# Kernel optimization log

Hardware: AMD Instinct MI355X
Metric: run time of the kernel (lower is better)

Reference implementation:

```python
import jax, jax.numpy as jnp
import numpy as np

N_QUBITS = 7
N_LAYERS = 2
DIM = 2 ** N_QUBITS  # 128
NORM_FACTOR = 1.0


def _cnot_gather_idx(n):
    # CNOT chain (0,1),(1,2),...,(n-2,n-1) plus wraparound (n-1,0).
    # new_state[x] = old_state[idx[x]]; apply gates in reverse to arange.
    gates = [(i, i + 1) for i in range(n - 1)] + [(n - 1, 0)]
    idx = np.arange(2 ** n)
    for c, t in reversed(gates):
        cbit = 1 << (n - 1 - c)  # pennylane wire 0 = most significant bit
        tbit = 1 << (n - 1 - t)
        idx = np.where((idx & cbit) > 0, idx ^ tbit, idx)
    return jnp.asarray(idx)

CNOT_IDX = _cnot_gather_idx(N_QUBITS)


def silu(x):
    return x * jax.nn.sigmoid(x)


def cayley(A_real, A_imag):
    # Hermitianize then Cayley transform -> unitary, per layer. [L,D,D]
    A = A_real.astype(jnp.complex64) + 1j * A_imag.astype(jnp.complex64)
    A = A + jnp.conj(jnp.swapaxes(A, -1, -2))
    I = jnp.eye(DIM, dtype=A.dtype)
    return jnp.matmul(A - 1j * I, jnp.linalg.inv(A + 1j * I))


def _single_qubit_gate(theta_x, theta_y):
    # combined G = RY(theta_y) @ RX(theta_x) applied to every qubit
    cx, sx = jnp.cos(theta_x / 2), jnp.sin(theta_x / 2)
    cy, sy = jnp.cos(theta_y / 2), jnp.sin(theta_y / 2)
    RX = jnp.stack([jnp.stack([cx + 0j, -1j * sx]), jnp.stack([-1j * sx, cx + 0j])])
    RY = jnp.stack([jnp.stack([cy + 0j, -sy + 0j]), jnp.stack([sy + 0j, cy + 0j])])
    return RY @ RX


def quantum_evolve(psi, coeffs, q_mats):
    # psi: [N, DIM] complex64 normalized state vectors
    N = psi.shape[0]
    for j in range(N_LAYERS):
        psi = psi @ q_mats[j].T  # QubitUnitary: new = U @ old
        G = _single_qubit_gate(coeffs[j, 0], coeffs[j, 1])
        psi = psi.reshape((N,) + (2,) * N_QUBITS)
        for ax in range(1, N_QUBITS + 1):
            psi = jnp.moveaxis(jnp.tensordot(G, psi, axes=((1,), (ax,))), 0, ax)
        psi = psi.reshape(N, DIM)
        psi = psi[:, CNOT_IDX]  # CNOT chain is a fixed basis permutation
    return psi


def setup_inputs() -> dict:
    key = jax.random.key(0)
    ks = jax.random.split(key, 16)
    N, E = 50000, 800000
    in_nf, hid, out_nf = 128, 128, 128
    h = jax.random.normal(ks[0], (N, in_nf), dtype=jnp.float32)
    edge_index = jax.random.randint(ks[1], (2, E), 0, N)
    s = 0.05
    W_e1 = jax.random.normal(ks[2], (2 * in_nf, hid), dtype=jnp.float32) * s
    b_e1 = jnp.zeros((hid,), dtype=jnp.float32)
    W_e2 = jax.random.normal(ks[3], (hid, hid), dtype=jnp.float32) * s
    b_e2 = jnp.zeros((hid,), dtype=jnp.float32)
    W_enc = jax.random.normal(ks[4], (hid + in_nf, DIM), dtype=jnp.float32) * s
    b_enc = jnp.zeros((DIM,), dtype=jnp.float32)
    coeffs = jax.random.normal(ks[5], (N_LAYERS, 2), dtype=jnp.float32) * 0.1
    A_real = jax.random.normal(ks[6], (N_LAYERS, DIM, DIM), dtype=jnp.float32) * 0.01
    A_imag = jax.random.normal(ks[7], (N_LAYERS, DIM, DIM), dtype=jnp.float32) * 0.01
    W_dec = jax.random.normal(ks[8], (DIM, out_nf), dtype=jnp.float32) * s
    b_dec = jnp.zeros((out_nf,), dtype=jnp.float32)
    return {"h": h, "edge_index": edge_index, "W_e1": W_e1, "b_e1": b_e1,
            "W_e2": W_e2, "b_e2": b_e2, "W_enc": W_enc, "b_enc": b_enc,
            "coeffs": coeffs, "A_real": A_real, "A_imag": A_imag,
            "W_dec": W_dec, "b_dec": b_dec}


def reference(h, edge_index, W_e1, b_e1, W_e2, b_e2, W_enc, b_enc,
              coeffs, A_real, A_imag, W_dec, b_dec):
    row, col = edge_index[0], edge_index[1]
    # edge model: mij = MLP([h_src, h_tgt])
    e = jnp.concatenate([h[row], h[col]], axis=1)  # [E, 2*in_nf]
    e = silu(e @ W_e1 + b_e1)
    edge_feat = silu(e @ W_e2 + b_e2)  # [E, hid]
    # node model: scatter-sum aggregation over destination `row`
    agg = jax.ops.segment_sum(edge_feat, row, num_segments=h.shape[0]) / NORM_FACTOR
    q_input = jnp.concatenate([h, agg], axis=1) @ W_enc + b_enc  # [N, DIM]
    norm = jnp.sqrt(jnp.sum(q_input ** 2, axis=1, keepdims=True) + 1e-12)
    psi = (q_input / norm).astype(jnp.complex64)
    q_mats = cayley(A_real, A_imag)  # [L, DIM, DIM] unitary
    psi = quantum_evolve(psi, coeffs, q_mats)
    out = h + (jnp.real(psi) @ W_dec + b_dec)
    return out, edge_feat
```

## Files before the change

### kernel.cpp

```cpp
#include <hip/hip_runtime.h>
#include <math.h>

#define N_NODES 50000
#define N_EDGES 800000

typedef __attribute__((ext_vector_type(8))) short bf16x8;
typedef __attribute__((ext_vector_type(4))) short bf16x4;
typedef __attribute__((ext_vector_type(2))) short shortx2;
typedef __attribute__((ext_vector_type(4))) float f32x4;

__device__ __forceinline__ float silu_f(float x) {
    float d = 1.0f + __expf(-x);
    return x * __builtin_amdgcn_rcpf(d);
}

__device__ __forceinline__ unsigned short f2bf(float x) {
    union { float f; unsigned u; } v; v.f = x;
    unsigned r = v.u + 0x7FFFu + ((v.u >> 16) & 1u);
    return (unsigned short)(r >> 16);
}

__device__ __forceinline__ void atomic_pk_add_bf16(short* addr, shortx2 v) {
    typedef shortx2 __attribute__((address_space(1)))* gp1;
    __builtin_amdgcn_global_atomic_fadd_v2bf16((gp1)(unsigned long long)addr, v);
}

__global__ __launch_bounds__(256) void prep_kernel(const float* __restrict__ h,
                                                   short* __restrict__ hbf,
                                                   const int* __restrict__ ei,
                                                   int* __restrict__ cnt,
                                                   const float* __restrict__ A_real,
                                                   const float* __restrict__ A_imag,
                                                   float* __restrict__ H,
                                                   float* __restrict__ X) {
    const int bid = blockIdx.x;
    const int t = threadIdx.x;
    if (bid < 3125) {
        int i = bid * 256 + t;
        const float4* h4 = (const float4*)h;
        float4 v0 = h4[i * 2], v1 = h4[i * 2 + 1];
        bf16x8 b;
        b[0] = (short)f2bf(v0.x); b[1] = (short)f2bf(v0.y);
        b[2] = (short)f2bf(v0.z); b[3] = (short)f2bf(v0.w);
        b[4] = (short)f2bf(v1.x); b[5] = (short)f2bf(v1.y);
        b[6] = (short)f2bf(v1.z); b[7] = (short)f2bf(v1.w);
        ((bf16x8*)hbf)[i] = b;
        atomicAdd(&cnt[ei[i]], 1);
    } else {
        int p = bid - 3125;
        int L = p >> 2, q4 = p & 3;
        const float* ar = A_real + L * 16384;
        const float* ai = A_imag + L * 16384;
        float* hre = H + L * 32768;
        float* him = hre + 16384;
        float* xre = X + L * 32768;
        float* xim = xre + 16384;
        for (int m = 0; m < 16; ++m) {
            int idx = q4 * 4096 + t + 256 * m;
            int i = idx >> 7, j = idx & 127;
            float hr = ar[idx] + ar[j * 128 + i];
            float hi = ai[idx] - ai[j * 128 + i];
            hre[idx] = hr;
            him[idx] = hi;
            xre[idx] = hr;
            xim[idx] = hi - (i == j ? 1.0f : 0.0f);
        }
    }
}

__device__ __forceinline__ void ns_t_body(int blk, int t,
                                          const float* __restrict__ H,
                                          const float* __restrict__ X,
                                          float* __restrict__ T) {
    const int L = blk >> 4;
    const int i = (blk & 15) * 8 + (t >> 7);
    const int j = t & 127;
    const float* hre = H + L * 32768;
    const float* him = hre + 16384;
    const float* xre = X + L * 32768;
    const float* xim = xre + 16384;
    float accr = 0.f, acci = 0.f;
    #pragma unroll 4
    for (int k = 0; k < 128; ++k) {
        float hr = hre[i * 128 + k], hi = him[i * 128 + k];
        float xr = xre[k * 128 + j], xi = xim[k * 128 + j];
        accr += hr * xr - hi * xi;
        acci += hr * xi + hi * xr;
    }
    T[L * 32768 + i * 128 + j]          = accr - xim[i * 128 + j];
    T[L * 32768 + 16384 + i * 128 + j]  = acci + xre[i * 128 + j];
}

__device__ __forceinline__ void ns_x_body(int blk, int t,
                                          const float* __restrict__ X,
                                          const float* __restrict__ T,
                                          float* __restrict__ Xout) {
    const int L = blk >> 4;
    const int i = (blk & 15) * 8 + (t >> 7);
    const int j = t & 127;
    const float* xre = X + L * 32768;
    const float* xim = xre + 16384;
    const float* tre = T + L * 32768;
    const float* tim = tre + 16384;
    float accr = 0.f, acci = 0.f;
    #pragma unroll 4
    for (int k = 0; k < 128; ++k) {
        float xr = xre[i * 128 + k], xi = xim[i * 128 + k];
        float tr = tre[k * 128 + j], ti = tim[k * 128 + j];
        accr += xr * tr - xi * ti;
        acci += xr * ti + xi * tr;
    }
    Xout[L * 32768 + i * 128 + j]          = 2.0f * xre[i * 128 + j] - accr;
    Xout[L * 32768 + 16384 + i * 128 + j]  = 2.0f * xim[i * 128 + j] - acci;
}

__global__ __launch_bounds__(1024) void nst_scan_kernel(const float* __restrict__ H,
                                                        const float* __restrict__ X,
                                                        float* __restrict__ T,
                                                        const int* __restrict__ cnt,
                                                        int* __restrict__ cursor) {
    const int bid = blockIdx.x;
    const int t = threadIdx.x;
    if (bid < 32) { ns_t_body(bid, t, H, X, T); return; }
    __shared__ int sA[1024];
    __shared__ int sB[1024];
    const int CH = 49;
    int s = 0;
    #pragma unroll 4
    for (int i = 0; i < CH; ++i) {
        int idx = t * CH + i;
        if (idx < N_NODES) s += cnt[idx];
    }
    sA[t] = s;
    __syncthreads();
    int* src = sA;
    int* dst = sB;
    for (int off = 1; off < 1024; off <<= 1) {
        int v = src[t];
        if (t >= off) v += src[t - off];
        dst[t] = v;
        __syncthreads();
        int* tmp = src; src = dst; dst = tmp;
    }
    int run = (t == 0) ? 0 : src[t - 1];
    for (int i = 0; i < CH; ++i) {
        int idx = t * CH + i;
        if (idx < N_NODES) {
            cursor[idx] = run;
            run += cnt[idx];
        }
    }
}

__global__ __launch_bounds__(1024) void fill_nsx_kernel(const int* __restrict__ ei,
                                                        int* __restrict__ cursor,
                                                        int* __restrict__ elist,
                                                        const float* __restrict__ X,
                                                        const float* __restrict__ T,
                                                        float* __restrict__ Xout) {
    const int bid = blockIdx.x;
    const int t = threadIdx.x;
    if (bid < 782) {
        int e = bid * 1024 + t;
        if (e < N_EDGES) {
            int slot = atomicAdd(&cursor[ei[e]], 1);
            elist[slot] = e;
        }
        return;
    }
    ns_x_body(bid - 782, t, X, T, Xout);
}

__global__ __launch_bounds__(1024) void ns_t_kernel(const float* __restrict__ H,
                                                    const float* __restrict__ X,
                                                    float* __restrict__ T) {
    ns_t_body(blockIdx.x, threadIdx.x, H, X, T);
}

__global__ __launch_bounds__(1024) void ns_x_kernel(const float* __restrict__ X,
                                                    const float* __restrict__ T,
                                                    float* __restrict__ Xout) {
    ns_x_body(blockIdx.x, threadIdx.x, X, T, Xout);
}

__global__ __launch_bounds__(1024) void gateperm_kernel(const float* __restrict__ X,
                                                        const float* __restrict__ coeffs,
                                                        float* __restrict__ Y) {
    __shared__ float Mre[128 * 129];
    __shared__ float Mim[128 * 129];
    const int L = blockIdx.x;
    const int t = threadIdx.x;
    const float* xre = X + L * 32768;
    const float* xim = xre + 16384;

    for (int q = 0; q < 16; ++q) {
        int idx = t + 1024 * q;
        int i = idx >> 7, j = idx & 127;
        Mre[i * 129 + j] = (i == j ? 1.0f : 0.0f) + 2.0f * xim[idx];
        Mim[i * 129 + j] = -2.0f * xre[idx];
    }
    __syncthreads();

    const float tx = coeffs[2 * L + 0] * 0.5f;
    const float ty = coeffs[2 * L + 1] * 0.5f;
    const float cx = cosf(tx), sx = sinf(tx), cy = cosf(ty), sy = sinf(ty);
    const float G00r = cx * cy, G00i = sx * sy;
    const float G01r = -cx * sy, G01i = -sx * cy;
    const float G10r = cx * sy, G10i = -sx * cy;
    const float G11r = cx * cy, G11i = -sx * sy;

    for (int st = 0; st < 7; ++st) {
        int b = 1 << st;
        #pragma unroll
        for (int p = 0; p < 8; ++p) {
            int pid = t + 1024 * p;
            int col = pid & 127, ph = pid >> 7;
            int i0 = ((ph >> st) << (st + 1)) | (ph & (b - 1));
            int i1 = i0 | b;
            float v0r = Mre[i0 * 129 + col], v0i = Mim[i0 * 129 + col];
            float v1r = Mre[i1 * 129 + col], v1i = Mim[i1 * 129 + col];
            Mre[i0 * 129 + col] = G00r * v0r - G00i * v0i + G01r * v1r - G01i * v1i;
            Mim[i0 * 129 + col] = G00r * v0i + G00i * v0r + G01r * v1i + G01i * v1r;
            Mre[i1 * 129 + col] = G10r * v0r - G10i * v0i + G11r * v1r - G11i * v1i;
            Mim[i1 * 129 + col] = G10r * v0i + G10i * v0r + G11r * v1i + G11i * v1r;
        }
        __syncthreads();
    }

    const int cs[7] = {6, 5, 4, 3, 2, 1, 0};
    const int ts[7] = {0, 6, 5, 4, 3, 2, 1};
    float* yre = Y + L * 32768;
    float* yim = yre + 16384;
    for (int q = 0; q < 16; ++q) {
        int idx = t + 1024 * q;
        int ii_ = idx >> 7, col = idx & 127;
        int s = ii_;
        #pragma unroll
        for (int m = 0; m < 7; ++m) {
            int cbit = 1 << (6 - cs[m]);
            int tbit = 1 << (6 - ts[m]);
            if (s & cbit) s ^= tbit;
        }
        yre[idx] = Mre[s * 129 + col];
        yim[idx] = Mim[s * 129 + col];
    }
}

__global__ __launch_bounds__(512) void combine1_kernel(const float* __restrict__ Y,
                                                       float* __restrict__ ReM) {
    __shared__ float q1r[16384];
    __shared__ float q1i[16384];
    const int t = threadIdx.x;
    const float* q1re = Y;
    const float* q1im = Y + 16384;
    const float* q2re = Y + 32768;
    const float* q2im = Y + 49152;
    for (int q = 0; q < 32; ++q) {
        q1r[t + 512 * q] = q1re[t + 512 * q];
        q1i[t + 512 * q] = q1im[t + 512 * q];
    }
    __syncthreads();
    int i = blockIdx.x * 4 + (t >> 7);
    int j = t & 127;
    float acc = 0.f;
    for (int k = 0; k < 128; ++k) {
        acc += q2re[i * 128 + k] * q1r[k * 128 + j] - q2im[i * 128 + k] * q1i[k * 128 + j];
    }
    ReM[i * 128 + j] = acc;
}

__global__ __launch_bounds__(512) void combine2_kernel(const float* __restrict__ ReM,
                                                       const float* __restrict__ W_dec,
                                                       short* __restrict__ Dt) {
    __shared__ float ml[16384];
    __shared__ float wl[16384];
    const int t = threadIdx.x;
    for (int q = 0; q < 32; ++q) {
        ml[t + 512 * q] = ReM[t + 512 * q];
        wl[t + 512 * q] = W_dec[t + 512 * q];
    }
    __syncthreads();
    int k = blockIdx.x * 4 + (t >> 7);
    int j = t & 127;
    float acc = 0.f;
    for (int i = 0; i < 128; ++i) {
        acc += ml[i * 128 + k] * wl[i * 128 + j];
    }
    Dt[j * 128 + k] = (short)f2bf(acc);
}

__global__ __launch_bounds__(768)
__attribute__((amdgpu_waves_per_eu(3, 3)))
void edge_kernel(const short* __restrict__ hbf,
                 const int* __restrict__ ei,
                 const int* __restrict__ elist,
                 const float* __restrict__ W_e1,
                 const float* __restrict__ b_e1,
                 const float* __restrict__ W_e2,
                 const float* __restrict__ b_e2,
                 float* __restrict__ ef_out,
                 short* __restrict__ agg_bf) {
    __shared__ short w1t[128 * 256];
    __shared__ short w2t[128 * 128];
    __shared__ short c1s[12][16 * 68];

    const int t = threadIdx.x;
    const int lane = t & 63;
    const int w = t >> 6;
    const int l15 = lane & 15;
    const int kg = lane >> 4;

    {
        const float4* w1_4 = (const float4*)W_e1;
        for (int idx4 = t; idx4 < 8192; idx4 += 768) {
            int k = idx4 >> 5, j4 = idx4 & 31;
            float4 v = w1_4[idx4];
            int j = j4 * 4;
            w1t[(j + 0) * 256 + (k ^ (((j + 0) & 7) << 3))] = (short)f2bf(v.x);
            w1t[(j + 1) * 256 + (k ^ (((j + 1) & 7) << 3))] = (short)f2bf(v.y);
            w1t[(j + 2) * 256 + (k ^ (((j + 2) & 7) << 3))] = (short)f2bf(v.z);
            w1t[(j + 3) * 256 + (k ^ (((j + 3) & 7) << 3))] = (short)f2bf(v.w);
        }
        const float4* w2_4 = (const float4*)W_e2;
        for (int idx4 = t; idx4 < 4096; idx4 += 768) {
            int k = idx4 >> 5, j4 = idx4 & 31;
            float4 v = w2_4[idx4];
            int j = j4 * 4;
            w2t[(j + 0) * 128 + (k ^ (((j + 0) & 7) << 3))] = (short)f2bf(v.x);
            w2t[(j + 1) * 128 + (k ^ (((j + 1) & 7) << 3))] = (short)f2bf(v.y);
            w2t[(j + 2) * 128 + (k ^ (((j + 2) & 7) << 3))] = (short)f2bf(v.z);
            w2t[(j + 3) * 128 + (k ^ (((j + 3) & 7) << 3))] = (short)f2bf(v.w);
        }
    }
    float b1v[8], b2v[8];
    #pragma unroll
    for (int nf = 0; nf < 8; ++nf) {
        b1v[nf] = b_e1[nf * 16 + l15];
        b2v[nf] = b_e2[nf * 16 + l15];
    }
    __syncthreads();

    const bf16x8* hb8 = (const bf16x8*)hbf;
    short* myc1 = &c1s[w][0];
    const int nt = N_EDGES / 16;
    const int TW = gridDim.x * 12;
    const int wvid = blockIdx.x * 12 + w;
    int tile = (int)(((long long)nt * wvid) / TW);
    const int tend = (int)(((long long)nt * (wvid + 1)) / TW);
    if (tile >= tend) return;

    int el = elist[tile * 16 + l15];
    int ri = ei[el];
    int ci = ei[N_EDGES + el];
    bf16x8 a1[8];
    #pragma unroll
    for (int s = 0; s < 4; ++s) a1[s] = hb8[(size_t)ri * 16 + s * 4 + kg];
    #pragma unroll
    for (int s = 0; s < 4; ++s) a1[4 + s] = hb8[(size_t)ci * 16 + s * 4 + kg];

    bool hn = (tile + 1 < tend);
    int eln = 0, rin = 0, cin = 0;
    if (hn) {
        eln = elist[(tile + 1) * 16 + l15];
        rin = ei[eln];
        cin = ei[N_EDGES + eln];
    }

    float runsum[8];
    #pragma unroll
    for (int nf = 0; nf < 8; ++nf) runsum[nf] = 0.f;

    for (;;) {
        bool hn2 = (tile + 2 < tend);
        int eln2 = 0, rin2 = 0, cin2 = 0;
        if (hn2) {
            eln2 = elist[(tile + 2) * 16 + l15];
            rin2 = ei[eln2];
            cin2 = ei[N_EDGES + eln2];
        }

        bf16x8 a1n[8];
        if (hn) {
            #pragma unroll
            for (int s = 0; s < 4; ++s) a1n[s] = hb8[(size_t)rin * 16 + s * 4 + kg];
            #pragma unroll
            for (int s = 0; s < 4; ++s) a1n[4 + s] = hb8[(size_t)cin * 16 + s * 4 + kg];
        }

        f32x4 acc[8];
        #pragma unroll
        for (int nf = 0; nf < 8; ++nf) acc[nf] = (f32x4){0.f, 0.f, 0.f, 0.f};
        #pragma unroll
        for (int s = 0; s < 8; ++s) {
            const int k0 = s * 32 + kg * 8;
            #pragma unroll
            for (int nf = 0; nf < 8; ++nf) {
                int brow = nf * 16 + l15;
                bf16x8 b = *(const bf16x8*)&w1t[brow * 256 + (k0 ^ ((brow & 7) << 3))];
                acc[nf] = __builtin_amdgcn_mfma_f32_16x16x32_bf16(a1[s], b, acc[nf], 0, 0, 0);
            }
        }

        f32x4 acc2[8];
        #pragma unroll
        for (int nf = 0; nf < 8; ++nf) acc2[nf] = (f32x4){0.f, 0.f, 0.f, 0.f};
        #pragma unroll
        for (int half = 0; half < 2; ++half) {
            #pragma unroll
            for (int nfh = 0; nfh < 4; ++nfh) {
                int nf = half * 4 + nfh;
                #pragma unroll
                for (int r = 0; r < 4; ++r) {
                    int row = kg * 4 + r;
                    int c = nfh * 16 + l15;
                    myc1[row * 68 + c] = (short)f2bf(silu_f(acc[nf][r] + b1v[nf]));
                }
            }
            #pragma unroll
            for (int s2l = 0; s2l < 2; ++s2l) {
                int k0h = s2l * 32 + kg * 8;
                int base = l15 * 68 + k0h;
                bf16x4 lo = *(const bf16x4*)&myc1[base];
                bf16x4 hi = *(const bf16x4*)&myc1[base + 4];
                bf16x8 a2;
                #pragma unroll
                for (int z = 0; z < 4; ++z) { a2[z] = lo[z]; a2[4 + z] = hi[z]; }
                int k0g = half * 64 + k0h;
                #pragma unroll
                for (int nf = 0; nf < 8; ++nf) {
                    int brow = nf * 16 + l15;
                    bf16x8 b = *(const bf16x8*)&w2t[brow * 128 + (k0g ^ ((brow & 7) << 3))];
                    acc2[nf] = __builtin_amdgcn_mfma_f32_16x16x32_bf16(a2, b, acc2[nf], 0, 0, 0);
                }
            }
        }

        int rw[4], ew[4];
        #pragma unroll
        for (int r = 0; r < 4; ++r) {
            rw[r] = __shfl(ri, kg * 4 + r);
            ew[r] = __shfl(el, kg * 4 + r);
        }
        int rwn0 = hn ? __shfl(rin, kg * 4) : -1;
        #pragma unroll
        for (int r = 0; r < 4; ++r) {
            float* efp = ef_out + (size_t)ew[r] * 128;
            #pragma unroll
            for (int nf = 0; nf < 8; ++nf) {
                int col = nf * 16 + l15;
                float v = silu_f(acc2[nf][r] + b2v[nf]);
                __builtin_nontemporal_store(v, efp + col);
                runsum[nf] += v;
            }
            bool end = (r < 3) ? (rw[r + 1] != rw[r]) : (rw[3] != rwn0);
            if (end) {
                short* agp = agg_bf + (size_t)rw[r] * 128;
                #pragma unroll
                for (int nf = 0; nf < 8; ++nf) {
                    float vn = __shfl_xor(runsum[nf], 1);
                    if ((l15 & 1) == 0) {
                        shortx2 pk;
                        pk.x = (short)f2bf(runsum[nf]);
                        pk.y = (short)f2bf(vn);
                        atomic_pk_add_bf16(agp + nf * 16 + l15, pk);
                    }
                    runsum[nf] = 0.f;
                }
            }
        }

        if (!hn) break;
        tile += 1;
        el = eln; ri = rin; ci = cin;
        #pragma unroll
        for (int s = 0; s < 8; ++s) a1[s] = a1n[s];
        hn = hn2; eln = eln2; rin = rin2; cin = cin2;
    }
}

__global__ __launch_bounds__(1024)
__attribute__((amdgpu_waves_per_eu(4, 4)))
void node_kernel(const short* __restrict__ hbf,
                 const short* __restrict__ agg_bf,
                 const float* __restrict__ W_enc,
                 const float* __restrict__ b_enc,
                 const short* __restrict__ Dt_bf,
                 const float* __restrict__ b_dec,
                 const float* __restrict__ h,
                 float* __restrict__ out) {
    __shared__ short wet[128 * 256];
    __shared__ short dtl[128 * 128];
    __shared__ short c1s[16][1024];

    const int t = threadIdx.x;
    const int lane = t & 63;
    const int w = t >> 6;
    const int l15 = lane & 15;
    const int kg = lane >> 4;

    {
        const float4* we4 = (const float4*)W_enc;
        for (int q = 0; q < 8; ++q) {
            int idx4 = t + 1024 * q;
            int k = idx4 >> 5, j4 = idx4 & 31;
            float4 v = we4[idx4];
            int j = j4 * 4;
            wet[(j + 0) * 256 + (k ^ (((j + 0) & 7) << 3))] = (short)f2bf(v.x);
            wet[(j + 1) * 256 + (k ^ (((j + 1) & 7) << 3))] = (short)f2bf(v.y);
            wet[(j + 2) * 256 + (k ^ (((j + 2) & 7) << 3))] = (short)f2bf(v.z);
            wet[(j + 3) * 256 + (k ^ (((j + 3) & 7) << 3))] = (short)f2bf(v.w);
        }
        const int4* s4 = (const int4*)Dt_bf;
        for (int q = 0; q < 2; ++q) {
            int idx4 = t + 1024 * q;
            int j = idx4 >> 4, c = idx4 & 15;
            int k0 = c * 8;
            int4 v = s4[idx4];
            *(int4*)&dtl[j * 128 + (k0 ^ ((j & 7) << 3))] = v;
        }
    }
    float bj1[8], bj2[8];
    #pragma unroll
    for (int nf = 0; nf < 8; ++nf) {
        bj1[nf] = b_enc[nf * 16 + l15];
        bj2[nf] = b_dec[nf * 16 + l15];
    }
    __syncthreads();

    const bf16x8* hb8 = (const bf16x8*)hbf;
    const bf16x8* ab8 = (const bf16x8*)agg_bf;
    short* myc1 = &c1s[w][0];
    const int nt = N_NODES / 16;
    const int tile = blockIdx.x * 16 + w;
    if (tile >= nt) return;

    const int node = tile * 16 + l15;
    bf16x8 a[8];
    #pragma unroll
    for (int s = 0; s < 4; ++s) a[s] = hb8[(size_t)node * 16 + s * 4 + kg];
    #pragma unroll
    for (int s = 0; s < 4; ++s) a[4 + s] = ab8[(size_t)node * 16 + s * 4 + kg];

    f32x4 acc[8];
    #pragma unroll
    for (int nf = 0; nf < 8; ++nf) acc[nf] = (f32x4){0.f, 0.f, 0.f, 0.f};
    #pragma unroll
    for (int s = 0; s < 8; ++s) {
        const int k0 = s * 32 + kg * 8;
        #pragma unroll
        for (int nf = 0; nf < 8; ++nf) {
            int brow = nf * 16 + l15;
            bf16x8 b = *(const bf16x8*)&wet[brow * 256 + (k0 ^ ((brow & 7) << 3))];
            acc[nf] = __builtin_amdgcn_mfma_f32_16x16x32_bf16(a[s], b, acc[nf], 0, 0, 0);
        }
    }

    float nr[4] = {0.f, 0.f, 0.f, 0.f};
    #pragma unroll
    for (int nf = 0; nf < 8; ++nf) {
        #pragma unroll
        for (int r = 0; r < 4; ++r) {
            acc[nf][r] += bj1[nf];
            nr[r] += acc[nf][r] * acc[nf][r];
        }
    }
    #pragma unroll
    for (int r = 0; r < 4; ++r) {
        nr[r] += __shfl_xor(nr[r], 1);
        nr[r] += __shfl_xor(nr[r], 2);
        nr[r] += __shfl_xor(nr[r], 4);
        nr[r] += __shfl_xor(nr[r], 8);
        nr[r] = 1.0f / sqrtf(nr[r] + 1e-12f);
    }

    f32x4 acc2[8];
    #pragma unroll
    for (int nf = 0; nf < 8; ++nf) acc2[nf] = (f32x4){0.f, 0.f, 0.f, 0.f};
    #pragma unroll
    for (int half = 0; half < 2; ++half) {
        #pragma unroll
        for (int nfh = 0; nfh < 4; ++nfh) {
            int nf = half * 4 + nfh;
            #pragma unroll
            for (int r = 0; r < 4; ++r) {
                int row = kg * 4 + r;
                int c = nfh * 16 + l15;
                myc1[row * 64 + (c ^ ((row & 7) << 3))] = (short)f2bf(acc[nf][r] * nr[r]);
            }
        }
        #pragma unroll
        for (int s2l = 0; s2l < 2; ++s2l) {
            int k0h = s2l * 32 + kg * 8;
            bf16x8 a2 = *(const bf16x8*)&myc1[l15 * 64 + (k0h ^ ((l15 & 7) << 3))];
            int k0g = half * 64 + k0h;
            #pragma unroll
            for (int nf = 0; nf < 8; ++nf) {
                int brow = nf * 16 + l15;
                bf16x8 b = *(const bf16x8*)&dtl[brow * 128 + (k0g ^ ((brow & 7) << 3))];
                acc2[nf] = __builtin_amdgcn_mfma_f32_16x16x32_bf16(a2, b, acc2[nf], 0, 0, 0);
            }
        }
    }

    #pragma unroll
    for (int r = 0; r < 4; ++r) {
        size_t rowb = (size_t)(tile * 16 + kg * 4 + r) * 128;
        #pragma unroll
        for (int nf = 0; nf < 8; ++nf) {
            int col = nf * 16 + l15;
            out[rowb + col] = h[rowb + col] + acc2[nf][r] + bj2[nf];
        }
    }
}

extern "C" void kernel_launch(void* const* d_in, const int* in_sizes, int n_in,
                              void* d_out, int out_size, void* d_ws, size_t ws_size,
                              hipStream_t stream) {
    const float* h      = (const float*)d_in[0];
    const int*   ei     = (const int*)d_in[1];
    const float* W_e1   = (const float*)d_in[2];
    const float* b_e1   = (const float*)d_in[3];
    const float* W_e2   = (const float*)d_in[4];
    const float* b_e2   = (const float*)d_in[5];
    const float* W_enc  = (const float*)d_in[6];
    const float* b_enc  = (const float*)d_in[7];
    const float* coeffs = (const float*)d_in[8];
    const float* A_real = (const float*)d_in[9];
    const float* A_imag = (const float*)d_in[10];
    const float* W_dec  = (const float*)d_in[11];
    const float* b_dec  = (const float*)d_in[12];

    float* out    = (float*)d_out;
    float* ef_out = out + (size_t)N_NODES * 128;

    short* agg_bf = (short*)d_ws;
    int*   cnt    = (int*)(agg_bf + (size_t)N_NODES * 128);
    short* h_bf   = (short*)(cnt + 50176);
    int*   cursor = (int*)(h_bf + (size_t)N_NODES * 128);
    int*   elist  = cursor + 50176;
    float* small  = (float*)(elist + N_EDGES);
    float* Ybuf   = small;
    float* ReM    = Ybuf + 65536;
    float* Hbuf   = ReM + 16384;
    float* Xa     = Hbuf + 65536;
    float* Xb     = Xa + 65536;
    float* Tbuf   = Xb + 65536;
    short* Dt_bf  = (short*)(Tbuf + 65536);

    hipMemsetAsync(agg_bf, 0, (size_t)N_NODES * 128 * sizeof(short) + 50176 * sizeof(int),
                   stream);

    prep_kernel<<<3133, 256, 0, stream>>>(h, h_bf, ei, cnt, A_real, A_imag, Hbuf, Xa);
    nst_scan_kernel<<<33, 1024, 0, stream>>>(Hbuf, Xa, Tbuf, cnt, cursor);
    fill_nsx_kernel<<<814, 1024, 0, stream>>>(ei, cursor, elist, Xa, Tbuf, Xb);
    ns_t_kernel<<<32, 1024, 0, stream>>>(Hbuf, Xb, Tbuf);
    ns_x_kernel<<<32, 1024, 0, stream>>>(Xb, Tbuf, Xa);

    gateperm_kernel<<<2, 1024, 0, stream>>>(Xa, coeffs, Ybuf);
    combine1_kernel<<<32, 512, 0, stream>>>(Ybuf, ReM);
    combine2_kernel<<<32, 512, 0, stream>>>(ReM, W_dec, Dt_bf);

    edge_kernel<<<256, 768, 0, stream>>>(h_bf, ei, elist, W_e1, b_e1, W_e2, b_e2,
                                         ef_out, agg_bf);

    node_kernel<<<196, 1024, 0, stream>>>(h_bf, agg_bf, W_enc, b_enc, Dt_bf, b_dec, h, out);
}
```

Before: 604.7 us.

## Store MLP weights in LDS as pre-swizzled MFMA fragments for linear loads

Edge and node kernels now lay out bf16 weights in shared memory in fragment order, indexed by (k-step, n-fragment, lane). Each B-operand read becomes a contiguous 16-byte load at lane offset, with no XOR swizzle address math. The edge kernel also issues the first GEMM before the next tile's gather loads. The node kernel switches its activation staging to the padded stride-68 layout used by the edge kernel. Costs are more complex staging stores and split 8-byte activation reads in the node kernel.

```diff
diff --git a/kernel.cpp b/kernel.cpp
--- a/kernel.cpp
+++ b/kernel.cpp
@@ -300,8 +300,8 @@
                  const float* __restrict__ b_e2,
                  float* __restrict__ ef_out,
                  short* __restrict__ agg_bf) {
-    __shared__ short w1t[128 * 256];
-    __shared__ short w2t[128 * 128];
+    __shared__ short w1f[64 * 64 * 8];
+    __shared__ short w2f[32 * 64 * 8];
     __shared__ short c1s[12][16 * 68];
 
     const int t = threadIdx.x;
@@ -315,21 +315,29 @@
         for (int idx4 = t; idx4 < 8192; idx4 += 768) {
             int k = idx4 >> 5, j4 = idx4 & 31;
             float4 v = w1_4[idx4];
-            int j = j4 * 4;
-            w1t[(j + 0) * 256 + (k ^ (((j + 0) & 7) << 3))] = (short)f2bf(v.x);
-            w1t[(j + 1) * 256 + (k ^ (((j + 1) & 7) << 3))] = (short)f2bf(v.y);
-            w1t[(j + 2) * 256 + (k ^ (((j + 2) & 7) << 3))] = (short)f2bf(v.z);
-            w1t[(j + 3) * 256 + (k ^ (((j + 3) & 7) << 3))] = (short)f2bf(v.w);
+            int s = k >> 5, kgs = (k >> 3) & 3, e = k & 7;
+            int fb = s * 8;
+            float vz[4] = {v.x, v.y, v.z, v.w};
+            #pragma unroll
+            for (int z = 0; z < 4; ++z) {
+                int j = j4 * 4 + z;
+                int nf = j >> 4, jl = j & 15;
+                w1f[((fb + nf) * 64 + kgs * 16 + jl) * 8 + e] = (short)f2bf(vz[z]);
+            }
         }
         const float4* w2_4 = (const float4*)W_e2;
         for (int idx4 = t; idx4 < 4096; idx4 += 768) {
             int k = idx4 >> 5, j4 = idx4 & 31;
             float4 v = w2_4[idx4];
-            int j = j4 * 4;
-            w2t[(j + 0) * 128 + (k ^ (((j + 0) & 7) << 3))] = (short)f2bf(v.x);
-            w2t[(j + 1) * 128 + (k ^ (((j + 1) & 7) << 3))] = (short)f2bf(v.y);
-            w2t[(j + 2) * 128 + (k ^ (((j + 2) & 7) << 3))] = (short)f2bf(v.z);
-            w2t[(j + 3) * 128 + (k ^ (((j + 3) & 7) << 3))] = (short)f2bf(v.w);
+            int s2 = k >> 5, kgs = (k >> 3) & 3, e = k & 7;
+            int fb = s2 * 8;
+            float vz[4] = {v.x, v.y, v.z, v.w};
+            #pragma unroll
+            for (int z = 0; z < 4; ++z) {
+                int j = j4 * 4 + z;
+                int nf = j >> 4, jl = j & 15;
+                w2f[((fb + nf) * 64 + kgs * 16 + jl) * 8 + e] = (short)f2bf(vz[z]);
+            }
         }
     }
     float b1v[8], b2v[8];
@@ -341,6 +349,8 @@
     __syncthreads();
 
     const bf16x8* hb8 = (const bf16x8*)hbf;
+    const bf16x8* w1v = (const bf16x8*)w1f;
+    const bf16x8* w2v = (const bf16x8*)w2f;
     short* myc1 = &c1s[w][0];
     const int nt = N_EDGES / 16;
     const int TW = gridDim.x * 12;
@@ -379,26 +389,24 @@
             cin2 = ei[N_EDGES + eln2];
         }
 
+        f32x4 acc[8];
+        #pragma unroll
+        for (int nf = 0; nf < 8; ++nf) acc[nf] = (f32x4){0.f, 0.f, 0.f, 0.f};
+        #pragma unroll
+        for (int s = 0; s < 8; ++s) {
+            #pragma unroll
+            for (int nf = 0; nf < 8; ++nf) {
+                bf16x8 b = w1v[(s * 8 + nf) * 64 + lane];
+                acc[nf] = __builtin_amdgcn_mfma_f32_16x16x32_bf16(a1[s], b, acc[nf], 0, 0, 0);
+            }
+        }
+
         bf16x8 a1n[8];
         if (hn) {
             #pragma unroll
             for (int s = 0; s < 4; ++s) a1n[s] = hb8[(size_t)rin * 16 + s * 4 + kg];
             #pragma unroll
             for (int s = 0; s < 4; ++s) a1n[4 + s] = hb8[(size_t)cin * 16 + s * 4 + kg];
-        }
-
-        f32x4 acc[8];
-        #pragma unroll
-        for (int nf = 0; nf < 8; ++nf) acc[nf] = (f32x4){0.f, 0.f, 0.f, 0.f};
-        #pragma unroll
-        for (int s = 0; s < 8; ++s) {
-            const int k0 = s * 32 + kg * 8;
-            #pragma unroll
-            for (int nf = 0; nf < 8; ++nf) {
-                int brow = nf * 16 + l15;
-                bf16x8 b = *(const bf16x8*)&w1t[brow * 256 + (k0 ^ ((brow & 7) << 3))];
-                acc[nf] = __builtin_amdgcn_mfma_f32_16x16x32_bf16(a1[s], b, acc[nf], 0, 0, 0);
-            }
         }
 
         f32x4 acc2[8];
@@ -425,11 +433,10 @@
                 bf16x8 a2;
                 #pragma unroll
                 for (int z = 0; z < 4; ++z) { a2[z] = lo[z]; a2[4 + z] = hi[z]; }
-                int k0g = half * 64 + k0h;
+                int s2 = half * 2 + s2l;
                 #pragma unroll
                 for (int nf = 0; nf < 8; ++nf) {
-                    int brow = nf * 16 + l15;
-                    bf16x8 b = *(const bf16x8*)&w2t[brow * 128 + (k0g ^ ((brow & 7) << 3))];
+                    bf16x8 b = w2v[(s2 * 8 + nf) * 64 + lane];
                     acc2[nf] = __builtin_amdgcn_mfma_f32_16x16x32_bf16(a2, b, acc2[nf], 0, 0, 0);
                 }
             }
@@ -488,9 +495,9 @@
                  const float* __restrict__ b_dec,
                  const float* __restrict__ h,
                  float* __restrict__ out) {
-    __shared__ short wet[128 * 256];
-    __shared__ short dtl[128 * 128];
-    __shared__ short c1s[16][1024];
+    __shared__ short wef[64 * 64 * 8];
+    __shared__ short dtf[32 * 64 * 8];
+    __shared__ short c1s[16][16 * 68];
 
     const int t = threadIdx.x;
     const int lane = t & 63;
@@ -500,23 +507,26 @@
 
     {
         const float4* we4 = (const float4*)W_enc;
-        for (int q = 0; q < 8; ++q) {
-            int idx4 = t + 1024 * q;
+        for (int idx4 = t; idx4 < 8192; idx4 += 1024) {
             int k = idx4 >> 5, j4 = idx4 & 31;
             float4 v = we4[idx4];
-            int j = j4 * 4;
-            wet[(j + 0) * 256 + (k ^ (((j + 0) & 7) << 3))] = (short)f2bf(v.x);
-            wet[(j + 1) * 256 + (k ^ (((j + 1) & 7) << 3))] = (short)f2bf(v.y);
-            wet[(j + 2) * 256 + (k ^ (((j + 2) & 7) << 3))] = (short)f2bf(v.z);
-            wet[(j + 3) * 256 + (k ^ (((j + 3) & 7) << 3))] = (short)f2bf(v.w);
-        }
-        const int4* s4 = (const int4*)Dt_bf;
-        for (int q = 0; q < 2; ++q) {
-            int idx4 = t + 1024 * q;
-            int j = idx4 >> 4, c = idx4 & 15;
-            int k0 = c * 8;
-            int4 v = s4[idx4];
-            *(int4*)&dtl[j * 128 + (k0 ^ ((j & 7) << 3))] = v;
+            int s = k >> 5, kgs = (k >> 3) & 3, e = k & 7;
+            int fb = s * 8;
+            float vz[4] = {v.x, v.y, v.z, v.w};
+            #pragma unroll
+            for (int z = 0; z < 4; ++z) {
+                int j = j4 * 4 + z;
+                int nf = j >> 4, jl = j & 15;
+                wef[((fb + nf) * 64 + kgs * 16 + jl) * 8 + e] = (short)f2bf(vz[z]);
+            }
+        }
+        const bf16x8* dt8 = (const bf16x8*)Dt_bf;
+        bf16x8* dtv = (bf16x8*)dtf;
+        for (int idx8 = t; idx8 < 2048; idx8 += 1024) {
+            int brow = idx8 >> 4, kslot = idx8 & 15;
+            int s2 = kslot >> 2, kgs = kslot & 3;
+            int nf = brow >> 4, jl = brow & 15;
+            dtv[(s2 * 8 + nf) * 64 + kgs * 16 + jl] = dt8[idx8];
         }
     }
     float bj1[8], bj2[8];
@@ -529,6 +539,8 @@
 
     const bf16x8* hb8 = (const bf16x8*)hbf;
     const bf16x8* ab8 = (const bf16x8*)agg_bf;
+    const bf16x8* wev = (const bf16x8*)wef;
+    const bf16x8* dtv = (const bf16x8*)dtf;
     short* myc1 = &c1s[w][0];
     const int nt = N_NODES / 16;
     const int tile = blockIdx.x * 16 + w;
@@ -546,11 +558,9 @@
     for (int nf = 0; nf < 8; ++nf) acc[nf] = (f32x4){0.f, 0.f, 0.f, 0.f};
     #pragma unroll
     for (int s = 0; s < 8; ++s) {
-        const int k0 = s * 32 + kg * 8;
         #pragma unroll
         for (int nf = 0; nf < 8; ++nf) {
-            int brow = nf * 16 + l15;
-            bf16x8 b = *(const bf16x8*)&wet[brow * 256 + (k0 ^ ((brow & 7) << 3))];
+            bf16x8 b = wev[(s * 8 + nf) * 64 + lane];
             acc[nf] = __builtin_amdgcn_mfma_f32_16x16x32_bf16(a[s], b, acc[nf], 0, 0, 0);
         }
     }
@@ -585,18 +595,22 @@
             for (int r = 0; r < 4; ++r) {
                 int row = kg * 4 + r;
                 int c = nfh * 16 + l15;
-                myc1[row * 64 + (c ^ ((row & 7) << 3))] = (short)f2bf(acc[nf][r] * nr[r]);
+                myc1[row * 68 + c] = (short)f2bf(acc[nf][r] * nr[r]);
             }
         }
         #pragma unroll
         for (int s2l = 0; s2l < 2; ++s2l) {
             int k0h = s2l * 32 + kg * 8;
-            bf16x8 a2 = *(const bf16x8*)&myc1[l15 * 64 + (k0h ^ ((l15 & 7) << 3))];
-            int k0g = half * 64 + k0h;
+            int base = l15 * 68 + k0h;
+            bf16x4 lo = *(const bf16x4*)&myc1[base];
+            bf16x4 hi = *(const bf16x4*)&myc1[base + 4];
+            bf16x8 a2;
+            #pragma unroll
+            for (int z = 0; z < 4; ++z) { a2[z] = lo[z]; a2[4 + z] = hi[z]; }
+            int s2 = half * 2 + s2l;
             #pragma unroll
             for (int nf = 0; nf < 8; ++nf) {
-                int brow = nf * 16 + l15;
-                bf16x8 b = *(const bf16x8*)&dtl[brow * 128 + (k0g ^ ((brow & 7) << 3))];
+                bf16x8 b = dtv[(s2 * 8 + nf) * 64 + lane];
                 acc2[nf] = __builtin_amdgcn_mfma_f32_16x16x32_bf16(a2, b, acc2[nf], 0, 0, 0);
             }
         }
```

New measurement: 593.6 us. No clear change (-1.8%).
